# Kernel tuning notes

Measured on AMD Instinct MI355X. Metric: run time of the kernel, lower is better.

The kernel has to match this reference:

```python
import jax, jax.numpy as jnp
import numpy as np
from jax import lax

B_SZ, C_IN, T_LEN = 8, 80, 1000
D_MODEL, D_STATE, D_CONV, EXPAND = 256, 16, 4, 2
D_INNER = EXPAND * D_MODEL
DT_RANK = D_MODEL // 16  # math.ceil(256/16) = 16
N_LABELS = 35


def setup_inputs() -> dict:
    key = jax.random.key(0)
    ks = jax.random.split(key, 12)
    s = lambda k, shape: (jax.random.normal(k, shape, jnp.float32) * 0.02)
    A_log = jnp.log(jnp.tile(jnp.arange(1, D_STATE + 1, dtype=jnp.float32), (D_INNER, 1)))
    return {
        "x": jax.random.normal(ks[0], (B_SZ, C_IN, T_LEN), jnp.float32),
        "proj_w": s(ks[1], (D_MODEL, C_IN)),
        "proj_b": jnp.zeros((D_MODEL,), jnp.float32),
        "in_proj_w": s(ks[2], (2 * D_INNER, D_MODEL)),
        "conv_w": s(ks[3], (D_INNER, D_CONV)),
        "conv_b": jnp.zeros((D_INNER,), jnp.float32),
        "x_proj_w": s(ks[4], (DT_RANK + 2 * D_STATE, D_INNER)),
        "dt_proj_w": s(ks[5], (D_INNER, DT_RANK)),
        "dt_proj_b": jax.random.uniform(ks[6], (D_INNER,), jnp.float32, -4.0, -2.0),
        "A_log": A_log,
        "D": jnp.ones((D_INNER,), jnp.float32),
        "out_proj_w": s(ks[7], (D_MODEL, D_INNER)),
        "fc_w": s(ks[8], (N_LABELS, D_MODEL)),
        "fc_b": jnp.zeros((N_LABELS,), jnp.float32),
    }


def _mamba(u, in_proj_w, conv_w, conv_b, x_proj_w, dt_proj_w, dt_proj_b, A_log, D, out_proj_w):
    # u: (B, L, d_model) -> (B, L, d_model)
    Bn, L, _ = u.shape
    xz = u @ in_proj_w.T                      # (B, L, 2*d_inner)
    xh, z = jnp.split(xz, 2, axis=-1)
    # causal depthwise conv along L
    xc = jnp.pad(xh.transpose(0, 2, 1), ((0, 0), (0, 0), (D_CONV - 1, 0)))  # (B, d_inner, L+pad)
    xh = lax.conv_general_dilated(xc, conv_w[:, None, :], (1,), 'VALID',
                                  feature_group_count=D_INNER)             # (B, d_inner, L)
    xh = jax.nn.silu(xh.transpose(0, 2, 1) + conv_b)                        # (B, L, d_inner)
    dbc = xh @ x_proj_w.T                                                   # (B, L, dt_rank+2*d_state)
    dt, Bm, Cm = jnp.split(dbc, [DT_RANK, DT_RANK + D_STATE], axis=-1)
    delta = jax.nn.softplus(dt @ dt_proj_w.T + dt_proj_b)                   # (B, L, d_inner)
    A = -jnp.exp(A_log)                                                     # (d_inner, d_state)
    deltaA = jnp.exp(delta[..., None] * A)                                  # (B, L, d_inner, d_state)
    deltaBu = delta[..., None] * Bm[:, :, None, :] * xh[..., None]          # (B, L, d_inner, d_state)

    def step(h, inp):
        dA_t, dBu_t, C_t = inp
        h = dA_t * h + dBu_t                    # (B, d_inner, d_state)
        y_t = jnp.einsum('bds,bs->bd', h, C_t)  # (B, d_inner)
        return h, y_t

    h0 = jnp.zeros((Bn, D_INNER, D_STATE), u.dtype)
    _, ys = lax.scan(step, h0,
                     (deltaA.transpose(1, 0, 2, 3),
                      deltaBu.transpose(1, 0, 2, 3),
                      Cm.transpose(1, 0, 2)))
    y = ys.transpose(1, 0, 2) + xh * D          # (B, L, d_inner)
    y = y * jax.nn.silu(z)
    return y @ out_proj_w.T                     # (B, L, d_model)


def reference(x, proj_w, proj_b, in_proj_w, conv_w, conv_b, x_proj_w,
              dt_proj_w, dt_proj_b, A_log, D, out_proj_w, fc_w, fc_b):
    # x: (B, input_dim, T) -> permute -> Linear -> (B, T, d_model)
    h = x.transpose(0, 2, 1) @ proj_w.T + proj_b
    # Mamba selective scan over the time axis (model permutes channel-first; math identical)
    y = _mamba(h, in_proj_w, conv_w, conv_b, x_proj_w, dt_proj_w, dt_proj_b,
               A_log, D, out_proj_w)            # (B, T, d_model)
    # dropout is identity at inference; mean over time (== mean(dim=2) on (B,d_model,T))
    pooled = y.mean(axis=1)                     # (B, d_model)
    return pooled @ fc_w.T + fc_b               # (B, n_labels)
```

## Files before the change

kernel.cpp:

```cpp
#include <hip/hip_runtime.h>
#include <math.h>


#define OFF_W1T    0
#define OFF_B1     81920
#define OFF_W2S    82944
#define OFF_AL2    100864
#define OFF_XH     109056
#define OFF_SZ     4205056
#define OFF_CHUNKA 8301056
#define OFF_ACC16  12495360
#define OFF_DBCP   12560896
#define OFF_YBAR   18878976
#define WS_FLOATS  18883072

#define CK_FLOATS 262144
#define CHUNK_BASE(ck) (OFF_CHUNKA + (ck) * CK_FLOATS)

__device__ __forceinline__ float silu_f(float v) {
  return v / (1.f + __expf(-v));
}

__global__ __launch_bounds__(256) void prep_w1t(const float* __restrict__ proj_w,
                                                const float* __restrict__ in_proj_w,
                                                float* __restrict__ ws) {
  const int nt = blockIdx.x;
  const int ct = blockIdx.y;
  const int n0 = nt * 64, c0 = ct * 16;
  __shared__ float Pl[16 * 68];
  __shared__ float Il[64 * 68];
  const int tid = threadIdx.x;
  const int ng = tid & 31, cg = tid >> 5;
  float acc[2][2] = {{0.f, 0.f}, {0.f, 0.f}};
  for (int kc = 0; kc < 256; kc += 64) {
    __syncthreads();
    for (int i = tid; i < 16 * 64; i += 256) {
      int k = i >> 4, c = i & 15;
      Pl[c * 68 + k] = proj_w[(kc + k) * 80 + c0 + c];
    }
    for (int i = tid; i < 64 * 64; i += 256) {
      int n = i >> 6, k = i & 63;
      Il[k * 68 + n] = in_proj_w[(n0 + n) * 256 + kc + k];
    }
    __syncthreads();
    for (int k = 0; k < 64; ++k) {
      float p0 = Pl[(cg * 2 + 0) * 68 + k];
      float p1 = Pl[(cg * 2 + 1) * 68 + k];
      float2 iv = *(const float2*)&Il[k * 68 + ng * 2];
      acc[0][0] = fmaf(p0, iv.x, acc[0][0]);
      acc[0][1] = fmaf(p0, iv.y, acc[0][1]);
      acc[1][0] = fmaf(p1, iv.x, acc[1][0]);
      acc[1][1] = fmaf(p1, iv.y, acc[1][1]);
    }
  }
  for (int r = 0; r < 2; ++r)
    for (int q = 0; q < 2; ++q)
      ws[OFF_W1T + (c0 + cg * 2 + r) * 1024 + n0 + ng * 2 + q] = acc[r][q];
}

__global__ __launch_bounds__(256) void prep_small(const float* __restrict__ proj_b,
                                                  const float* __restrict__ in_proj_w,
                                                  const float* __restrict__ fc_w,
                                                  const float* __restrict__ out_proj_w,
                                                  const float* __restrict__ A_log,
                                                  float* __restrict__ ws) {
  int idx = blockIdx.x * 256 + threadIdx.x;
  if (idx < 1024) {
    float s = 0.f;
    for (int m = 0; m < 256; ++m) s = fmaf(in_proj_w[idx * 256 + m], proj_b[m], s);
    ws[OFF_B1 + idx] = s;
  } else if (idx < 1024 + 17920) {
    int j = idx - 1024;
    int n = j / 512, d = j - n * 512;
    float s = 0.f;
    for (int m = 0; m < 256; ++m) s = fmaf(fc_w[n * 256 + m], out_proj_w[m * 512 + d], s);
    ws[OFF_W2S + j] = s * 1e-3f;
  } else if (idx < 1024 + 17920 + 8192) {
    int j = idx - (1024 + 17920);
    ws[OFF_AL2 + j] = -expf(A_log[j]);
  }
}

__global__ __launch_bounds__(256) void k1_xz(const float* __restrict__ x,
                                             const float* __restrict__ conv_w,
                                             const float* __restrict__ conv_b,
                                             float* __restrict__ ws) {
  const int nt  = blockIdx.x;
  const int tcb = blockIdx.y;
  const int b   = blockIdx.z;
  const int tid = threadIdx.x;
  const int lane = tid & 63;
  const int wv   = tid >> 6;
  const int t0b  = tcb * 32;
  const int tw0  = t0b + wv * 8;

  __shared__ __align__(16) float xs[80 * 36];
  for (int i = tid; i < 2880; i += 256) {
    int k = i / 36, j = i - k * 36;
    int t = t0b - 4 + j;
    float v = 0.f;
    if (t >= 0 && t < 1000) v = x[(b * 80 + k) * 1000 + t];
    xs[i] = v;
  }
  __syncthreads();

  const int nb = nt * 256 + lane;
  float acc[4][12];
#pragma unroll
  for (int c = 0; c < 4; ++c) {
    float b1v = ws[OFF_B1 + nb + 64 * c];
#pragma unroll
    for (int j = 0; j < 12; ++j) acc[c][j] = b1v;
  }

  const float* __restrict__ w1t = ws + OFF_W1T;
  const int woff = wv * 8;
  for (int k = 0; k < 80; ++k) {
    float wreg[4];
#pragma unroll
    for (int c = 0; c < 4; ++c)
      wreg[c] = w1t[k * 1024 + nb + 64 * c];
    float xv[12];
    *(float4*)&xv[0] = *(const float4*)&xs[k * 36 + woff + 0];
    *(float4*)&xv[4] = *(const float4*)&xs[k * 36 + woff + 4];
    *(float4*)&xv[8] = *(const float4*)&xs[k * 36 + woff + 8];
#pragma unroll
    for (int c = 0; c < 4; ++c)
#pragma unroll
      for (int j = 0; j < 12; ++j)
        acc[c][j] = fmaf(xv[j], wreg[c], acc[c][j]);
  }

  if (tcb == 0 && wv == 0) {
#pragma unroll
    for (int c = 0; c < 4; ++c) {
      acc[c][0] = 0.f; acc[c][1] = 0.f; acc[c][2] = 0.f; acc[c][3] = 0.f;
    }
  }

  if (nt < 2) {
#pragma unroll
    for (int c = 0; c < 4; ++c) {
      const int d = nb + 64 * c;
      const float4 cw = *(const float4*)&conv_w[d * 4];
      const float cb = conv_b[d];
#pragma unroll
      for (int i = 0; i < 8; ++i) {
        int t = tw0 + i;
        if (t < 1000) {
          float v = cb;
          v = fmaf(cw.x, acc[c][i + 1], v);
          v = fmaf(cw.y, acc[c][i + 2], v);
          v = fmaf(cw.z, acc[c][i + 3], v);
          v = fmaf(cw.w, acc[c][i + 4], v);
          ws[OFF_XH + (b * 1000 + t) * 512 + d] = silu_f(v);
        }
      }
    }
  } else {
#pragma unroll
    for (int c = 0; c < 4; ++c) {
      const int d0 = nb - 512 + 64 * c;
#pragma unroll
      for (int i = 0; i < 8; ++i) {
        int t = tw0 + i;
        if (t < 1000)
          ws[OFF_SZ + (b * 1000 + t) * 512 + d0] = silu_f(acc[c][i + 4]);
      }
    }
  }
}

__global__ __launch_bounds__(256) void k2b_dbc(const float* __restrict__ x_proj_w,
                                               float* __restrict__ ws) {
  const int row0 = blockIdx.x * 16;
  const int ks   = blockIdx.y;
  const int k0   = ks * 256;
  __shared__ float Xl[16 * 68];
  __shared__ float Wl[48 * 68];
  const int tid = threadIdx.x;
  const int ng = tid & 15, rg = tid >> 4;
  float acc[3] = {0.f, 0.f, 0.f};
  for (int kc = 0; kc < 256; kc += 64) {
    __syncthreads();
    for (int i = tid; i < 16 * 64; i += 256) {
      int r = i >> 6, c = i & 63;
      Xl[r * 68 + c] = ws[OFF_XH + (row0 + r) * 512 + k0 + kc + c];
    }
    for (int i = tid; i < 48 * 64; i += 256) {
      int r = i >> 6, c = i & 63;
      Wl[r * 68 + c] = x_proj_w[r * 512 + k0 + kc + c];
    }
    __syncthreads();
    for (int c = 0; c < 64; c += 4) {
      float4 xa = *(const float4*)&Xl[rg * 68 + c];
      float4 w0 = *(const float4*)&Wl[(ng * 3 + 0) * 68 + c];
      float4 w1 = *(const float4*)&Wl[(ng * 3 + 1) * 68 + c];
      float4 w2 = *(const float4*)&Wl[(ng * 3 + 2) * 68 + c];
      acc[0] += xa.x*w0.x + xa.y*w0.y + xa.z*w0.z + xa.w*w0.w;
      acc[1] += xa.x*w1.x + xa.y*w1.y + xa.z*w1.z + xa.w*w1.w;
      acc[2] += xa.x*w2.x + xa.y*w2.y + xa.z*w2.z + xa.w*w2.w;
    }
  }
  for (int n = 0; n < 3; ++n)
    ws[OFF_DBCP + ks * 384000 + (row0 + rg) * 48 + ng * 3 + n] = acc[n];
}

__global__ __launch_bounds__(512) void k3_scan1(const float* __restrict__ dt_proj_w,
                                                const float* __restrict__ dt_proj_b,
                                                float* __restrict__ ws) {
  const int dg = blockIdx.x;
  const int ck = blockIdx.y;
  const int b  = blockIdx.z;
  const int tid = threadIdx.x;
  const int lane = tid & 63;
  const int wv = tid >> 6;
  const int d = dg * 64 + lane;
  const int nt = (ck < 8) ? 63 : 62;
  const int tstart = (ck < 8) ? 63 * ck : 62 * ck + 8;
  const int rowbase = b * 1000 + tstart;

  __shared__ __align__(16) float dbcl[63 * 48];
  __shared__ float dlt[63 * 64];
  for (int i = tid; i < nt * 48; i += 512)
    dbcl[i] = ws[OFF_DBCP + rowbase * 48 + i] +
              ws[OFF_DBCP + 384000 + rowbase * 48 + i];
  __syncthreads();

  {
    const float4* wp = (const float4*)(dt_proj_w + d * 16);
    const float4 w0 = wp[0], w1 = wp[1], w2 = wp[2], w3 = wp[3];
    const float bias = dt_proj_b[d];
    const int tend = (wv * 8 + 8 < nt) ? wv * 8 + 8 : nt;
    for (int tt = wv * 8; tt < tend; ++tt) {
      const float* dr = &dbcl[tt * 48];
      float lin = bias;
      lin = fmaf(dr[0],  w0.x, lin); lin = fmaf(dr[1],  w0.y, lin);
      lin = fmaf(dr[2],  w0.z, lin); lin = fmaf(dr[3],  w0.w, lin);
      lin = fmaf(dr[4],  w1.x, lin); lin = fmaf(dr[5],  w1.y, lin);
      lin = fmaf(dr[6],  w1.z, lin); lin = fmaf(dr[7],  w1.w, lin);
      lin = fmaf(dr[8],  w2.x, lin); lin = fmaf(dr[9],  w2.y, lin);
      lin = fmaf(dr[10], w2.z, lin); lin = fmaf(dr[11], w2.w, lin);
      lin = fmaf(dr[12], w3.x, lin); lin = fmaf(dr[13], w3.y, lin);
      lin = fmaf(dr[14], w3.z, lin); lin = fmaf(dr[15], w3.w, lin);
      dlt[tt * 64 + lane] = fmaxf(lin, 0.f) + log1pf(__expf(-fabsf(lin)));
    }
  }
  __syncthreads();

  const float2 av = *(const float2*)&ws[OFF_AL2 + d * 16 + wv * 2];
  const float a0 = av.x, a1 = av.y;
  const float* __restrict__ xhp = ws + OFF_XH + rowbase * 512 + d;
  const float* __restrict__ szp = ws + OFF_SZ + rowbase * 512 + d;
  float h0 = 0.f, h1 = 0.f, cp0 = 1.f, cp1 = 1.f;
  float S10 = 0.f, S11 = 0.f, S20 = 0.f, S21 = 0.f, xacc = 0.f;
#pragma unroll 4
  for (int i = 0; i < nt; ++i) {
    float del = dlt[i * 64 + lane];
    float xh  = xhp[i * 512];
    float sz  = szp[i * 512];
    float2 bB = *(const float2*)&dbcl[i * 48 + 16 + wv * 2];
    float2 bC = *(const float2*)&dbcl[i * 48 + 32 + wv * 2];
    float du = del * xh;
    xacc = fmaf(xh, sz, xacc);
    float e0 = __expf(del * a0), e1 = __expf(del * a1);
    cp0 *= e0; cp1 *= e1;
    h0 = fmaf(e0, h0, du * bB.x);
    h1 = fmaf(e1, h1, du * bB.y);
    float cs0 = bC.x * sz, cs1 = bC.y * sz;
    S10 = fmaf(h0, cs0, S10); S11 = fmaf(h1, cs1, S11);
    S20 = fmaf(cp0, cs0, S20); S21 = fmaf(cp1, cs1, S21);
  }
  {
    const int cbase = CHUNK_BASE(ck);
    const int s = wv * 2;
    int idx = (b * 16 + s) * 512 + d;
    *(float4*)&ws[cbase + idx * 4] = make_float4(cp0, h0, S10, S20);
    *(float4*)&ws[cbase + (idx + 512) * 4] = make_float4(cp1, h1, S11, S21);
  }
  if (wv == 0) ws[OFF_ACC16 + (ck * 8 + b) * 512 + d] = xacc;
}

__global__ __launch_bounds__(256) void k4_scan2(const float* __restrict__ Dvec,
                                                float* __restrict__ ws) {
  const int dg = blockIdx.x;
  const int b  = blockIdx.y;
  const int tid = threadIdx.x;
  const int dl = tid & 15, s = tid >> 4;
  const int d = dg * 16 + dl;
  const int lane = tid & 63, wv = tid >> 6;
  float h = 0.f, y = 0.f;
#pragma unroll
  for (int k = 0; k < 16; ++k) {
    const float4 f = *(const float4*)&ws[CHUNK_BASE(k) + ((b * 16 + s) * 512 + d) * 4];
    y = fmaf(f.w, h, y + f.z);
    h = fmaf(f.x, h, f.y);
  }
  y += __shfl_xor(y, 16);
  y += __shfl_xor(y, 32);
  __shared__ float ys[4][16];
  if (lane < 16) ys[wv][dl] = y;
  __syncthreads();
  if (tid < 16) {
    float yt = ys[0][tid] + ys[1][tid] + ys[2][tid] + ys[3][tid];
    float acc = 0.f;
#pragma unroll
    for (int k = 0; k < 16; ++k) acc += ws[OFF_ACC16 + (k * 8 + b) * 512 + dg * 16 + tid];
    int dd = dg * 16 + tid;
    ws[OFF_YBAR + b * 512 + dd] = yt + Dvec[dd] * acc;
  }
}

__global__ __launch_bounds__(64) void k5_out(const float* __restrict__ fc_b,
                                             const float* __restrict__ ws,
                                             float* __restrict__ out) {
  const int b = blockIdx.x;
  const int n = threadIdx.x;
  if (n >= 35) return;
  const float* yb = ws + OFF_YBAR + b * 512;
  const float* w  = ws + OFF_W2S + n * 512;
  float sum = 0.f;
#pragma unroll 8
  for (int k = 0; k < 512; ++k) sum = fmaf(yb[k], w[k], sum);
  out[b * 35 + n] = sum + fc_b[n];
}

extern "C" void kernel_launch(void* const* d_in, const int* in_sizes, int n_in,
                              void* d_out, int out_size, void* d_ws, size_t ws_size,
                              hipStream_t stream) {
  const float* x          = (const float*)d_in[0];
  const float* proj_w     = (const float*)d_in[1];
  const float* proj_b     = (const float*)d_in[2];
  const float* in_proj_w  = (const float*)d_in[3];
  const float* conv_w     = (const float*)d_in[4];
  const float* conv_b     = (const float*)d_in[5];
  const float* x_proj_w   = (const float*)d_in[6];
  const float* dt_proj_w  = (const float*)d_in[7];
  const float* dt_proj_b  = (const float*)d_in[8];
  const float* A_log      = (const float*)d_in[9];
  const float* Dvec       = (const float*)d_in[10];
  const float* out_proj_w = (const float*)d_in[11];
  const float* fc_w       = (const float*)d_in[12];
  const float* fc_b       = (const float*)d_in[13];
  float* ws  = (float*)d_ws;
  float* out = (float*)d_out;
  if (ws_size < (size_t)WS_FLOATS * sizeof(float)) return;

  prep_w1t  <<<dim3(16, 5),    256, 0, stream>>>(proj_w, in_proj_w, ws);
  prep_small<<<106,            256, 0, stream>>>(proj_b, in_proj_w, fc_w, out_proj_w, A_log, ws);
  k1_xz     <<<dim3(4, 32, 8), 256, 0, stream>>>(x, conv_w, conv_b, ws);
  k2b_dbc   <<<dim3(500, 2),   256, 0, stream>>>(x_proj_w, ws);
  k3_scan1  <<<dim3(8, 16, 8), 512, 0, stream>>>(dt_proj_w, dt_proj_b, ws);
  k4_scan2  <<<dim3(32, 8),    256, 0, stream>>>(Dvec, ws);
  k5_out    <<<8,              64,  0, stream>>>(fc_b, ws, out);
}
```

Before: 157.6 us.

## Merge prep kernels, register-prefetch and specialize k1 projection, vectorize dt loads

Combines the two weight-prep kernels into one launch to save a kernel launch. Restructures k1_xz into a templated body with scalar accumulators, software-prefetched weights and a z-half variant that skips the three left-halo FMAs it never uses, and adds a launch_bounds occupancy hint. Also vectorizes the dt row loads in the scan kernel into float4 shared-memory reads. The aim is fewer instructions and less latency in the input projection, though the occupancy hint may cause register spills.

```diff
diff --git a/kernel.cpp b/kernel.cpp
--- a/kernel.cpp
+++ b/kernel.cpp
@@ -21,78 +21,135 @@
   return v / (1.f + __expf(-v));
 }
 
-__global__ __launch_bounds__(256) void prep_w1t(const float* __restrict__ proj_w,
+__global__ __launch_bounds__(256) void prep_all(const float* __restrict__ proj_w,
+                                                const float* __restrict__ proj_b,
                                                 const float* __restrict__ in_proj_w,
+                                                const float* __restrict__ fc_w,
+                                                const float* __restrict__ out_proj_w,
+                                                const float* __restrict__ A_log,
                                                 float* __restrict__ ws) {
-  const int nt = blockIdx.x;
-  const int ct = blockIdx.y;
-  const int n0 = nt * 64, c0 = ct * 16;
-  __shared__ float Pl[16 * 68];
-  __shared__ float Il[64 * 68];
   const int tid = threadIdx.x;
-  const int ng = tid & 31, cg = tid >> 5;
-  float acc[2][2] = {{0.f, 0.f}, {0.f, 0.f}};
-  for (int kc = 0; kc < 256; kc += 64) {
-    __syncthreads();
-    for (int i = tid; i < 16 * 64; i += 256) {
-      int k = i >> 4, c = i & 15;
-      Pl[c * 68 + k] = proj_w[(kc + k) * 80 + c0 + c];
-    }
-    for (int i = tid; i < 64 * 64; i += 256) {
-      int n = i >> 6, k = i & 63;
-      Il[k * 68 + n] = in_proj_w[(n0 + n) * 256 + kc + k];
-    }
-    __syncthreads();
-    for (int k = 0; k < 64; ++k) {
-      float p0 = Pl[(cg * 2 + 0) * 68 + k];
-      float p1 = Pl[(cg * 2 + 1) * 68 + k];
-      float2 iv = *(const float2*)&Il[k * 68 + ng * 2];
-      acc[0][0] = fmaf(p0, iv.x, acc[0][0]);
-      acc[0][1] = fmaf(p0, iv.y, acc[0][1]);
-      acc[1][0] = fmaf(p1, iv.x, acc[1][0]);
-      acc[1][1] = fmaf(p1, iv.y, acc[1][1]);
-    }
-  }
-  for (int r = 0; r < 2; ++r)
-    for (int q = 0; q < 2; ++q)
-      ws[OFF_W1T + (c0 + cg * 2 + r) * 1024 + n0 + ng * 2 + q] = acc[r][q];
-}
-
-__global__ __launch_bounds__(256) void prep_small(const float* __restrict__ proj_b,
-                                                  const float* __restrict__ in_proj_w,
-                                                  const float* __restrict__ fc_w,
-                                                  const float* __restrict__ out_proj_w,
-                                                  const float* __restrict__ A_log,
-                                                  float* __restrict__ ws) {
-  int idx = blockIdx.x * 256 + threadIdx.x;
-  if (idx < 1024) {
-    float s = 0.f;
-    for (int m = 0; m < 256; ++m) s = fmaf(in_proj_w[idx * 256 + m], proj_b[m], s);
-    ws[OFF_B1 + idx] = s;
-  } else if (idx < 1024 + 17920) {
-    int j = idx - 1024;
-    int n = j / 512, d = j - n * 512;
-    float s = 0.f;
-    for (int m = 0; m < 256; ++m) s = fmaf(fc_w[n * 256 + m], out_proj_w[m * 512 + d], s);
-    ws[OFF_W2S + j] = s * 1e-3f;
-  } else if (idx < 1024 + 17920 + 8192) {
-    int j = idx - (1024 + 17920);
-    ws[OFF_AL2 + j] = -expf(A_log[j]);
-  }
-}
-
-__global__ __launch_bounds__(256) void k1_xz(const float* __restrict__ x,
-                                             const float* __restrict__ conv_w,
-                                             const float* __restrict__ conv_b,
-                                             float* __restrict__ ws) {
-  const int nt  = blockIdx.x;
-  const int tcb = blockIdx.y;
-  const int b   = blockIdx.z;
+  if (blockIdx.x < 80) {
+    const int nt = blockIdx.x / 5;
+    const int ct = blockIdx.x % 5;
+    const int n0 = nt * 64, c0 = ct * 16;
+    __shared__ float Pl[16 * 68];
+    __shared__ float Il[64 * 68];
+    const int ng = tid & 31, cg = tid >> 5;
+    float acc[2][2] = {{0.f, 0.f}, {0.f, 0.f}};
+    for (int kc = 0; kc < 256; kc += 64) {
+      __syncthreads();
+      for (int i = tid; i < 16 * 64; i += 256) {
+        int k = i >> 4, c = i & 15;
+        Pl[c * 68 + k] = proj_w[(kc + k) * 80 + c0 + c];
+      }
+      for (int i = tid; i < 64 * 64; i += 256) {
+        int n = i >> 6, k = i & 63;
+        Il[k * 68 + n] = in_proj_w[(n0 + n) * 256 + kc + k];
+      }
+      __syncthreads();
+      for (int k = 0; k < 64; ++k) {
+        float p0 = Pl[(cg * 2 + 0) * 68 + k];
+        float p1 = Pl[(cg * 2 + 1) * 68 + k];
+        float2 iv = *(const float2*)&Il[k * 68 + ng * 2];
+        acc[0][0] = fmaf(p0, iv.x, acc[0][0]);
+        acc[0][1] = fmaf(p0, iv.y, acc[0][1]);
+        acc[1][0] = fmaf(p1, iv.x, acc[1][0]);
+        acc[1][1] = fmaf(p1, iv.y, acc[1][1]);
+      }
+    }
+    for (int r = 0; r < 2; ++r)
+      for (int q = 0; q < 2; ++q)
+        ws[OFF_W1T + (c0 + cg * 2 + r) * 1024 + n0 + ng * 2 + q] = acc[r][q];
+  } else {
+    int idx = (blockIdx.x - 80) * 256 + tid;
+    if (idx < 1024) {
+      float s = 0.f;
+      for (int m = 0; m < 256; ++m) s = fmaf(in_proj_w[idx * 256 + m], proj_b[m], s);
+      ws[OFF_B1 + idx] = s;
+    } else if (idx < 1024 + 17920) {
+      int j = idx - 1024;
+      int n = j / 512, d = j - n * 512;
+      float s = 0.f;
+      for (int m = 0; m < 256; ++m) s = fmaf(fc_w[n * 256 + m], out_proj_w[m * 512 + d], s);
+      ws[OFF_W2S + j] = s * 1e-3f;
+    } else if (idx < 1024 + 17920 + 8192) {
+      int j = idx - (1024 + 17920);
+      ws[OFF_AL2 + j] = -expf(A_log[j]);
+    }
+  }
+}
+
+
+__device__ __forceinline__ void k1_epil_h(int d, int b, int tw0,
+    const float* __restrict__ conv_w, const float* __restrict__ conv_b,
+    float* __restrict__ ws, bool zeroL,
+    float a1, float a2, float a3, float a4, float a5, float a6,
+    float a7, float a8, float a9, float a10, float a11) {
+  if (zeroL) { a1 = 0.f; a2 = 0.f; a3 = 0.f; }
+  const float4 cw = *(const float4*)&conv_w[d * 4];
+  const float cb = conv_b[d];
+  float s[11] = {a1, a2, a3, a4, a5, a6, a7, a8, a9, a10, a11};
+#pragma unroll
+  for (int i = 0; i < 8; ++i) {
+    float v = cb;
+    v = fmaf(cw.x, s[i + 0], v);
+    v = fmaf(cw.y, s[i + 1], v);
+    v = fmaf(cw.z, s[i + 2], v);
+    v = fmaf(cw.w, s[i + 3], v);
+    int t = tw0 + i;
+    if (t < 1000) ws[OFF_XH + (b * 1000 + t) * 512 + d] = silu_f(v);
+  }
+}
+
+__device__ __forceinline__ void k1_epil_z(int d0, int b, int tw0,
+    float* __restrict__ ws,
+    float a4, float a5, float a6, float a7, float a8, float a9,
+    float a10, float a11) {
+  float s[8] = {a4, a5, a6, a7, a8, a9, a10, a11};
+#pragma unroll
+  for (int i = 0; i < 8; ++i) {
+    int t = tw0 + i;
+    if (t < 1000) ws[OFF_SZ + (b * 1000 + t) * 512 + d0] = silu_f(s[i]);
+  }
+}
+
+#define K1_DECL(c)                                                          \
+  float A##c##1, A##c##2, A##c##3, A##c##4, A##c##5, A##c##6, A##c##7,      \
+        A##c##8, A##c##9, A##c##10, A##c##11;                               \
+  {                                                                         \
+    const float b1v = ws[OFF_B1 + nb + 64 * (c)];                           \
+    A##c##1 = b1v; A##c##2 = b1v; A##c##3 = b1v; A##c##4 = b1v;             \
+    A##c##5 = b1v; A##c##6 = b1v; A##c##7 = b1v; A##c##8 = b1v;             \
+    A##c##9 = b1v; A##c##10 = b1v; A##c##11 = b1v;                          \
+  }
+
+#define K1_FMA(c, W)                                                        \
+  if (CONVHALF) {                                                           \
+    A##c##1 = fmaf(x1, (W), A##c##1);                                       \
+    A##c##2 = fmaf(x2, (W), A##c##2);                                       \
+    A##c##3 = fmaf(x3, (W), A##c##3);                                       \
+  }                                                                         \
+  A##c##4  = fmaf(x4,  (W), A##c##4);                                       \
+  A##c##5  = fmaf(x5,  (W), A##c##5);                                       \
+  A##c##6  = fmaf(x6,  (W), A##c##6);                                       \
+  A##c##7  = fmaf(x7,  (W), A##c##7);                                       \
+  A##c##8  = fmaf(x8,  (W), A##c##8);                                       \
+  A##c##9  = fmaf(x9,  (W), A##c##9);                                       \
+  A##c##10 = fmaf(x10, (W), A##c##10);                                      \
+  A##c##11 = fmaf(x11, (W), A##c##11);
+
+template <bool CONVHALF>
+__device__ __forceinline__ void k1_body(const float* __restrict__ x,
+                                        const float* __restrict__ conv_w,
+                                        const float* __restrict__ conv_b,
+                                        float* __restrict__ ws,
+                                        int nt, int tcb, int b) {
   const int tid = threadIdx.x;
   const int lane = tid & 63;
-  const int wv   = tid >> 6;
-  const int t0b  = tcb * 32;
-  const int tw0  = t0b + wv * 8;
+  const int wv = tid >> 6;
+  const int t0b = tcb * 32;
+  const int tw0 = t0b + wv * 8;
 
   __shared__ __align__(16) float xs[80 * 36];
   for (int i = tid; i < 2880; i += 256) {
@@ -105,70 +162,59 @@
   __syncthreads();
 
   const int nb = nt * 256 + lane;
-  float acc[4][12];
-#pragma unroll
-  for (int c = 0; c < 4; ++c) {
-    float b1v = ws[OFF_B1 + nb + 64 * c];
-#pragma unroll
-    for (int j = 0; j < 12; ++j) acc[c][j] = b1v;
-  }
-
-  const float* __restrict__ w1t = ws + OFF_W1T;
+  K1_DECL(0) K1_DECL(1) K1_DECL(2) K1_DECL(3)
+
+  const float* __restrict__ wp = ws + OFF_W1T + nb;
   const int woff = wv * 8;
+  float w0n = wp[0], w1n = wp[64], w2n = wp[128], w3n = wp[192];
   for (int k = 0; k < 80; ++k) {
-    float wreg[4];
-#pragma unroll
-    for (int c = 0; c < 4; ++c)
-      wreg[c] = w1t[k * 1024 + nb + 64 * c];
-    float xv[12];
-    *(float4*)&xv[0] = *(const float4*)&xs[k * 36 + woff + 0];
-    *(float4*)&xv[4] = *(const float4*)&xs[k * 36 + woff + 4];
-    *(float4*)&xv[8] = *(const float4*)&xs[k * 36 + woff + 8];
-#pragma unroll
-    for (int c = 0; c < 4; ++c)
-#pragma unroll
-      for (int j = 0; j < 12; ++j)
-        acc[c][j] = fmaf(xv[j], wreg[c], acc[c][j]);
-  }
-
-  if (tcb == 0 && wv == 0) {
-#pragma unroll
-    for (int c = 0; c < 4; ++c) {
-      acc[c][0] = 0.f; acc[c][1] = 0.f; acc[c][2] = 0.f; acc[c][3] = 0.f;
-    }
-  }
-
-  if (nt < 2) {
-#pragma unroll
-    for (int c = 0; c < 4; ++c) {
-      const int d = nb + 64 * c;
-      const float4 cw = *(const float4*)&conv_w[d * 4];
-      const float cb = conv_b[d];
-#pragma unroll
-      for (int i = 0; i < 8; ++i) {
-        int t = tw0 + i;
-        if (t < 1000) {
-          float v = cb;
-          v = fmaf(cw.x, acc[c][i + 1], v);
-          v = fmaf(cw.y, acc[c][i + 2], v);
-          v = fmaf(cw.z, acc[c][i + 3], v);
-          v = fmaf(cw.w, acc[c][i + 4], v);
-          ws[OFF_XH + (b * 1000 + t) * 512 + d] = silu_f(v);
-        }
-      }
-    }
+    const float c0 = w0n, c1 = w1n, c2 = w2n, c3 = w3n;
+    if (k < 79) {
+      const float* wn = wp + (k + 1) * 1024;
+      w0n = wn[0]; w1n = wn[64]; w2n = wn[128]; w3n = wn[192];
+    }
+    float x1, x2, x3;
+    if (CONVHALF) {
+      float4 xa = *(const float4*)&xs[k * 36 + woff];
+      x1 = xa.y; x2 = xa.z; x3 = xa.w;
+    } else {
+      x1 = 0.f; x2 = 0.f; x3 = 0.f;
+    }
+    float4 xb = *(const float4*)&xs[k * 36 + woff + 4];
+    float4 xc = *(const float4*)&xs[k * 36 + woff + 8];
+    const float x4 = xb.x, x5 = xb.y, x6 = xb.z, x7 = xb.w;
+    const float x8 = xc.x, x9 = xc.y, x10 = xc.z, x11 = xc.w;
+    K1_FMA(0, c0) K1_FMA(1, c1) K1_FMA(2, c2) K1_FMA(3, c3)
+  }
+
+  const bool zeroL = (tcb == 0 && wv == 0);
+  if (CONVHALF) {
+    k1_epil_h(nb + 0,   b, tw0, conv_w, conv_b, ws, zeroL,
+              A01, A02, A03, A04, A05, A06, A07, A08, A09, A010, A011);
+    k1_epil_h(nb + 64,  b, tw0, conv_w, conv_b, ws, zeroL,
+              A11, A12, A13, A14, A15, A16, A17, A18, A19, A110, A111);
+    k1_epil_h(nb + 128, b, tw0, conv_w, conv_b, ws, zeroL,
+              A21, A22, A23, A24, A25, A26, A27, A28, A29, A210, A211);
+    k1_epil_h(nb + 192, b, tw0, conv_w, conv_b, ws, zeroL,
+              A31, A32, A33, A34, A35, A36, A37, A38, A39, A310, A311);
   } else {
-#pragma unroll
-    for (int c = 0; c < 4; ++c) {
-      const int d0 = nb - 512 + 64 * c;
-#pragma unroll
-      for (int i = 0; i < 8; ++i) {
-        int t = tw0 + i;
-        if (t < 1000)
-          ws[OFF_SZ + (b * 1000 + t) * 512 + d0] = silu_f(acc[c][i + 4]);
-      }
-    }
-  }
+    const int d0 = nb - 512;
+    k1_epil_z(d0 + 0,   b, tw0, ws, A04, A05, A06, A07, A08, A09, A010, A011);
+    k1_epil_z(d0 + 64,  b, tw0, ws, A14, A15, A16, A17, A18, A19, A110, A111);
+    k1_epil_z(d0 + 128, b, tw0, ws, A24, A25, A26, A27, A28, A29, A210, A211);
+    k1_epil_z(d0 + 192, b, tw0, ws, A34, A35, A36, A37, A38, A39, A310, A311);
+  }
+}
+
+__global__ __launch_bounds__(256, 2) void k1_xz(const float* __restrict__ x,
+                                                const float* __restrict__ conv_w,
+                                                const float* __restrict__ conv_b,
+                                                float* __restrict__ ws) {
+  const int nt  = blockIdx.x;
+  const int tcb = blockIdx.y;
+  const int b   = blockIdx.z;
+  if (nt < 2) k1_body<true >(x, conv_w, conv_b, ws, nt, tcb, b);
+  else        k1_body<false>(x, conv_w, conv_b, ws, nt, tcb, b);
 }
 
 __global__ __launch_bounds__(256) void k2b_dbc(const float* __restrict__ x_proj_w,
@@ -234,15 +280,19 @@
     const int tend = (wv * 8 + 8 < nt) ? wv * 8 + 8 : nt;
     for (int tt = wv * 8; tt < tend; ++tt) {
       const float* dr = &dbcl[tt * 48];
+      float4 q0 = *(const float4*)(dr + 0);
+      float4 q1 = *(const float4*)(dr + 4);
+      float4 q2 = *(const float4*)(dr + 8);
+      float4 q3 = *(const float4*)(dr + 12);
       float lin = bias;
-      lin = fmaf(dr[0],  w0.x, lin); lin = fmaf(dr[1],  w0.y, lin);
-      lin = fmaf(dr[2],  w0.z, lin); lin = fmaf(dr[3],  w0.w, lin);
-      lin = fmaf(dr[4],  w1.x, lin); lin = fmaf(dr[5],  w1.y, lin);
-      lin = fmaf(dr[6],  w1.z, lin); lin = fmaf(dr[7],  w1.w, lin);
-      lin = fmaf(dr[8],  w2.x, lin); lin = fmaf(dr[9],  w2.y, lin);
-      lin = fmaf(dr[10], w2.z, lin); lin = fmaf(dr[11], w2.w, lin);
-      lin = fmaf(dr[12], w3.x, lin); lin = fmaf(dr[13], w3.y, lin);
-      lin = fmaf(dr[14], w3.z, lin); lin = fmaf(dr[15], w3.w, lin);
+      lin = fmaf(q0.x, w0.x, lin); lin = fmaf(q0.y, w0.y, lin);
+      lin = fmaf(q0.z, w0.z, lin); lin = fmaf(q0.w, w0.w, lin);
+      lin = fmaf(q1.x, w1.x, lin); lin = fmaf(q1.y, w1.y, lin);
+      lin = fmaf(q1.z, w1.z, lin); lin = fmaf(q1.w, w1.w, lin);
+      lin = fmaf(q2.x, w2.x, lin); lin = fmaf(q2.y, w2.y, lin);
+      lin = fmaf(q2.z, w2.z, lin); lin = fmaf(q2.w, w2.w, lin);
+      lin = fmaf(q3.x, w3.x, lin); lin = fmaf(q3.y, w3.y, lin);
+      lin = fmaf(q3.z, w3.z, lin); lin = fmaf(q3.w, w3.w, lin);
       dlt[tt * 64 + lane] = fmaxf(lin, 0.f) + log1pf(__expf(-fabsf(lin)));
     }
   }
@@ -346,8 +396,8 @@
   float* out = (float*)d_out;
   if (ws_size < (size_t)WS_FLOATS * sizeof(float)) return;
 
-  prep_w1t  <<<dim3(16, 5),    256, 0, stream>>>(proj_w, in_proj_w, ws);
-  prep_small<<<106,            256, 0, stream>>>(proj_b, in_proj_w, fc_w, out_proj_w, A_log, ws);
+  prep_all  <<<186,            256, 0, stream>>>(proj_w, proj_b, in_proj_w, fc_w,
+                                                 out_proj_w, A_log, ws);
   k1_xz     <<<dim3(4, 32, 8), 256, 0, stream>>>(x, conv_w, conv_b, ws);
   k2b_dbc   <<<dim3(500, 2),   256, 0, stream>>>(x_proj_w, ws);
   k3_scan1  <<<dim3(8, 16, 8), 512, 0, stream>>>(dt_proj_w, dt_proj_b, ws);
```

Result: faster. 149.4 us (-5.2%).
